# Optimization experiments

Measured on AMD Instinct MI355X. Metric: run time of the kernel, lower is better.

Reference implementation:

```python
import jax, jax.numpy as jnp
import numpy as np

D = 768
H = 12
DH = D // H


def setup_inputs() -> dict:
    key = jax.random.key(0)
    ks = jax.random.split(key, 7)
    B, S = 8, 1024
    sequences = jax.random.normal(ks[0], (B, S, D), dtype=jnp.float32)
    # per-head Linear params: weight [H, DH, DH] (torch Linear convention y = x W^T + b), bias [H, DH]
    scale = 1.0 / np.sqrt(DH)
    Wq = jax.random.uniform(ks[1], (H, DH, DH), jnp.float32, -scale, scale)
    Wk = jax.random.uniform(ks[2], (H, DH, DH), jnp.float32, -scale, scale)
    Wv = jax.random.uniform(ks[3], (H, DH, DH), jnp.float32, -scale, scale)
    bq = jax.random.uniform(ks[4], (H, DH), jnp.float32, -scale, scale)
    bk = jax.random.uniform(ks[5], (H, DH), jnp.float32, -scale, scale)
    bv = jax.random.uniform(ks[6], (H, DH), jnp.float32, -scale, scale)
    return {"sequences": sequences, "Wq": Wq, "Wk": Wk, "Wv": Wv,
            "bq": bq, "bk": bk, "bv": bv}


def reference(sequences, Wq, Wk, Wv, bq, bk, bv):
    B, S, _ = sequences.shape
    x = sequences.reshape(B, S, H, DH)  # head slices along feature dim
    # torch Linear: y = x @ W.T + b  ->  einsum over last dim of W
    Q = jnp.einsum('bshd,hed->bshe', x, Wq) + bq
    K = jnp.einsum('bshd,hed->bshe', x, Wk) + bk
    V = jnp.einsum('bshd,hed->bshe', x, Wv) + bv
    scores = jnp.einsum('bshe,bthe->bhst', Q, K) / np.sqrt(DH).astype(np.float32)
    attn = jax.nn.softmax(scores, axis=-1)  # [B,H,S,S]
    out = jnp.einsum('bhst,bthd->bshd', attn, V)
    return out.reshape(B, S, H * DH)
```

## Files before the change

### kernel.cpp

```cpp
#include <hip/hip_runtime.h>

#define NH 12
#define DHEAD 64
#define DMODEL 768
#define SEQ 1024
#define NBH 96

typedef _Float16 h8 __attribute__((ext_vector_type(8)));
typedef _Float16 h4 __attribute__((ext_vector_type(4)));
typedef __fp16   fp16x2 __attribute__((ext_vector_type(2)));
typedef float f32x4 __attribute__((ext_vector_type(4)));


__global__ __launch_bounds__(256) void proj_kernel(
    const float* __restrict__ x,
    const float* __restrict__ Wq, const float* __restrict__ Wk,
    const float* __restrict__ Wv,
    const float* __restrict__ bq, const float* __restrict__ bk,
    const float* __restrict__ bv,
    _Float16* __restrict__ Qf, _Float16* __restrict__ Kf,
    _Float16* __restrict__ Vf)
{
    __shared__ _Float16 xh[128][72];
    __shared__ _Float16 yh[128][72];

    const int h    = blockIdx.y;
    const int mtx  = blockIdx.z;
    const int tid  = threadIdx.x;
    const int row0 = blockIdx.x * 128;
    const int lane = tid & 63;
    const int w    = tid >> 6;
    const int g    = lane >> 4;
    const int r    = lane & 15;

    const int b    = row0 >> 10;
    const int bh   = b * NH + h;
    const int s16b = (row0 & 1023) >> 4;
    const int s32b = (row0 & 1023) >> 5;

#pragma unroll
    for (int p = 0; p < 8; ++p) {
        const int rr = p * 16 + (tid >> 4);
        const int c4 = (tid & 15) * 4;
        float4 v = *(const float4*)(x + (size_t)(row0 + rr) * DMODEL
                                      + h * DHEAD + c4);
        h4 o = { (_Float16)v.x, (_Float16)v.y, (_Float16)v.z, (_Float16)v.w };
        *(h4*)(&xh[rr][c4]) = o;
    }

    const float* W    = (mtx == 0 ? Wq : (mtx == 1 ? Wk : Wv)) + h * DHEAD * DHEAD;
    const float* bias = (mtx == 0 ? bq : (mtx == 1 ? bk : bv)) + h * DHEAD;
    const float  ws   = (mtx == 0) ? 0.125f * 1.44269504f : 1.0f;

    h8 bf[4][2];
    float bcol[4];
#pragma unroll
    for (int n = 0; n < 4; ++n) {
        const float* Wr = W + (n * 16 + r) * DHEAD;
#pragma unroll
        for (int hf = 0; hf < 2; ++hf) {
            const float* p = Wr + hf * 32 + g * 8;
            float4 w0 = *(const float4*)(p);
            float4 w1 = *(const float4*)(p + 4);
            h8 o = { (_Float16)(w0.x * ws), (_Float16)(w0.y * ws),
                     (_Float16)(w0.z * ws), (_Float16)(w0.w * ws),
                     (_Float16)(w1.x * ws), (_Float16)(w1.y * ws),
                     (_Float16)(w1.z * ws), (_Float16)(w1.w * ws) };
            bf[n][hf] = o;
        }
        bcol[n] = bias[n * 16 + r] * ws;
    }
    __syncthreads();

#pragma unroll
    for (int gg = 0; gg < 2; ++gg) {
        const int gi = w + gg * 4;
        const h8 af0 = *(const h8*)(&xh[gi * 16 + r][g * 8]);
        const h8 af1 = *(const h8*)(&xh[gi * 16 + r][32 + g * 8]);
#pragma unroll
        for (int n = 0; n < 4; ++n) {
            f32x4 d = { bcol[n], bcol[n], bcol[n], bcol[n] };
            d = __builtin_amdgcn_mfma_f32_16x16x32_f16(af0, bf[n][0], d, 0, 0, 0);
            d = __builtin_amdgcn_mfma_f32_16x16x32_f16(af1, bf[n][1], d, 0, 0, 0);
#pragma unroll
            for (int reg = 0; reg < 4; ++reg)
                yh[gi * 16 + g * 4 + reg][n * 16 + r] = (_Float16)d[reg];
        }
    }
    __syncthreads();

    if (mtx < 2) {
        const int s16l = tid >> 5;
        const int lx   = tid & 31;
        h8* dstb = (h8*)(mtx == 0 ? Qf : Kf)
                 + ((size_t)(bh * 64 + s16b + s16l)) * 128;
#pragma unroll
        for (int hf = 0; hf < 2; ++hf)
#pragma unroll
            for (int li = 0; li < 2; ++li) {
                const int ln  = lx + li * 32;
                const int gg2 = ln >> 4, rr2 = ln & 15;
                h8 v = *(const h8*)(&yh[s16l * 16 + rr2][hf * 32 + gg2 * 8]);
                dstb[hf * 64 + ln] = v;
            }
    } else {
        const int s32l = tid >> 6;
        const int t    = (tid >> 4) & 3;
        const int li   = tid & 15;
        h8 wv[4];
#pragma unroll
        for (int k = 0; k < 4; ++k) {
            const int ln  = li * 4 + k;
            const int gg2 = ln >> 4, rr2 = ln & 15;
#pragma unroll
            for (int j = 0; j < 4; ++j) {
                wv[k][j]     = yh[s32l * 32 +      gg2 * 4 + j][t * 16 + rr2];
                wv[k][j + 4] = yh[s32l * 32 + 16 + gg2 * 4 + j][t * 16 + rr2];
            }
        }
        h8* dst = (h8*)Vf
                + (((size_t)(bh * 32 + s32b + s32l)) * 4 + t) * 64 + li * 4;
#pragma unroll
        for (int k = 0; k < 4; ++k) dst[k] = wv[k];
    }
}

__global__ __launch_bounds__(256, 4) void attn_kernel(
    const _Float16* __restrict__ Qf, const _Float16* __restrict__ Kf,
    const _Float16* __restrict__ Vf, float* __restrict__ out)
{
    __shared__ _Float16 kbuf[4][2048];
    __shared__ _Float16 vbuf[4][2048];

    const int orig    = blockIdx.x;
    const int logical = (orig & 7) * 96 + (orig >> 3);
    const int bh      = logical >> 3;
    const int qblk    = logical & 7;
    const int tid  = threadIdx.x;
    const int lane = tid & 63;
    const int w    = tid >> 6;
    const int g    = lane >> 4;
    const int r    = lane & 15;

    const h8* Qb = (const h8*)Qf + (size_t)bh * 64 * 128;
    const h8* Kb = (const h8*)Kf + (size_t)bh * 64 * 128;
    const h8* Vb = (const h8*)Vf + (size_t)bh * 32 * 256;

    const int q16_0 = qblk * 8 + w * 2;

    h8 qf[2][2];
#pragma unroll
    for (int qg = 0; qg < 2; ++qg) {
        qf[qg][0] = Qb[(q16_0 + qg) * 128 + lane];
        qf[qg][1] = Qb[(q16_0 + qg) * 128 + 64 + lane];
    }
    asm volatile("s_waitcnt vmcnt(0)" ::: "memory");

    f32x4 ot[2][4] = {};
    float lsum[2] = {};

#define STAGE(c, buf)                                                         \
    {                                                                         \
        const h8* gk = Kb + (size_t)(c) * 256 + w * 64 + lane;                \
        const h8* gv = Vb + (size_t)(c) * 256 + w * 64 + lane;                \
        __builtin_amdgcn_global_load_lds(                                     \
            (const __attribute__((address_space(1))) void*)gk,                \
            (__attribute__((address_space(3))) void*)(&kbuf[buf][w * 512]),   \
            16, 0, 0);                                                        \
        __builtin_amdgcn_global_load_lds(                                     \
            (const __attribute__((address_space(1))) void*)gv,                \
            (__attribute__((address_space(3))) void*)(&vbuf[buf][w * 512]),   \
            16, 0, 0);                                                        \
    }

#define CHUNK(c, VM, DOSTAGE)                                                 \
    {                                                                         \
        if (DOSTAGE) STAGE((c) + 2, ((c) + 2) & 3)                            \
        asm volatile("s_waitcnt vmcnt(" #VM ")" ::: "memory");                \
        __builtin_amdgcn_s_barrier();                                         \
        const int cur = (c) & 3;                                              \
        __builtin_amdgcn_s_setprio(1);                                        \
        h8 kr0[2], kr1[2];                                                    \
        kr0[0] = *(const h8*)(&kbuf[cur][0 * 512 + lane * 8]);                \
        kr0[1] = *(const h8*)(&kbuf[cur][1 * 512 + lane * 8]);                \
        kr1[0] = *(const h8*)(&kbuf[cur][2 * 512 + lane * 8]);                \
        kr1[1] = *(const h8*)(&kbuf[cur][3 * 512 + lane * 8]);                \
        f32x4 s[2][2];                                                        \
        _Pragma("unroll")                                                     \
        for (int qg = 0; qg < 2; ++qg) {                                      \
            s[qg][0] = __builtin_amdgcn_mfma_f32_16x16x32_f16(                \
                kr0[0], qf[qg][0], (f32x4){0.f, 0.f, 0.f, 0.f}, 0, 0, 0);     \
            s[qg][0] = __builtin_amdgcn_mfma_f32_16x16x32_f16(                \
                kr0[1], qf[qg][1], s[qg][0], 0, 0, 0);                        \
            s[qg][1] = __builtin_amdgcn_mfma_f32_16x16x32_f16(                \
                kr1[0], qf[qg][0], (f32x4){0.f, 0.f, 0.f, 0.f}, 0, 0, 0);     \
            s[qg][1] = __builtin_amdgcn_mfma_f32_16x16x32_f16(                \
                kr1[1], qf[qg][1], s[qg][1], 0, 0, 0);                        \
        }                                                                     \
        h8 up[2];                                                             \
        _Pragma("unroll")                                                     \
        for (int qg = 0; qg < 2; ++qg) {                                      \
            float p0 = __builtin_amdgcn_exp2f(s[qg][0][0]);                   \
            float p1 = __builtin_amdgcn_exp2f(s[qg][0][1]);                   \
            float p2 = __builtin_amdgcn_exp2f(s[qg][0][2]);                   \
            float p3 = __builtin_amdgcn_exp2f(s[qg][0][3]);                   \
            float p4 = __builtin_amdgcn_exp2f(s[qg][1][0]);                   \
            float p5 = __builtin_amdgcn_exp2f(s[qg][1][1]);                   \
            float p6 = __builtin_amdgcn_exp2f(s[qg][1][2]);                   \
            float p7 = __builtin_amdgcn_exp2f(s[qg][1][3]);                   \
            lsum[qg] += ((p0 + p1) + (p2 + p3)) + ((p4 + p5) + (p6 + p7));    \
            union { fp16x2 v2[4]; h8 v8; } u;                                 \
            u.v2[0] = __builtin_amdgcn_cvt_pkrtz(p0, p1);                     \
            u.v2[1] = __builtin_amdgcn_cvt_pkrtz(p2, p3);                     \
            u.v2[2] = __builtin_amdgcn_cvt_pkrtz(p4, p5);                     \
            u.v2[3] = __builtin_amdgcn_cvt_pkrtz(p6, p7);                     \
            up[qg] = u.v8;                                                    \
        }                                                                     \
        _Pragma("unroll")                                                     \
        for (int t = 0; t < 4; ++t) {                                         \
            h8 vr = *(const h8*)(&vbuf[cur][t * 512 + lane * 8]);             \
            ot[0][t] = __builtin_amdgcn_mfma_f32_16x16x32_f16(                \
                vr, up[0], ot[0][t], 0, 0, 0);                                \
            ot[1][t] = __builtin_amdgcn_mfma_f32_16x16x32_f16(                \
                vr, up[1], ot[1][t], 0, 0, 0);                                \
        }                                                                     \
        __builtin_amdgcn_s_setprio(0);                                        \
    }

    STAGE(0, 0)
    STAGE(1, 1)

    CHUNK(0, 4, 1)  CHUNK(1, 4, 1)  CHUNK(2, 4, 1)  CHUNK(3, 4, 1)
    CHUNK(4, 4, 1)  CHUNK(5, 4, 1)  CHUNK(6, 4, 1)  CHUNK(7, 4, 1)
    CHUNK(8, 4, 1)  CHUNK(9, 4, 1)  CHUNK(10, 4, 1) CHUNK(11, 4, 1)
    CHUNK(12, 4, 1) CHUNK(13, 4, 1) CHUNK(14, 4, 1) CHUNK(15, 4, 1)
    CHUNK(16, 4, 1) CHUNK(17, 4, 1) CHUNK(18, 4, 1) CHUNK(19, 4, 1)
    CHUNK(20, 4, 1) CHUNK(21, 4, 1) CHUNK(22, 4, 1) CHUNK(23, 4, 1)
    CHUNK(24, 4, 1) CHUNK(25, 4, 1) CHUNK(26, 4, 1) CHUNK(27, 4, 1)
    CHUNK(28, 4, 1) CHUNK(29, 4, 1) CHUNK(30, 2, 0) CHUNK(31, 0, 0)
#undef CHUNK
#undef STAGE

    const int b = bh / NH, h = bh % NH;
#pragma unroll
    for (int qg = 0; qg < 2; ++qg) {
        float l = lsum[qg];
        l += __shfl_xor(l, 16);
        l += __shfl_xor(l, 32);
        const float inv = 1.0f / l;
        float* op = out + ((size_t)b * SEQ + (q16_0 + qg) * 16 + r) * DMODEL
                  + h * DHEAD + g * 4;
#pragma unroll
        for (int t = 0; t < 4; ++t) {
            float4 res = { ot[qg][t][0] * inv, ot[qg][t][1] * inv,
                           ot[qg][t][2] * inv, ot[qg][t][3] * inv };
            *(float4*)(op + t * 16) = res;
        }
    }
}

extern "C" void kernel_launch(void* const* d_in, const int* in_sizes, int n_in,
                              void* d_out, int out_size, void* d_ws, size_t ws_size,
                              hipStream_t stream)
{
    const float* x  = (const float*)d_in[0];
    const float* Wq = (const float*)d_in[1];
    const float* Wk = (const float*)d_in[2];
    const float* Wv = (const float*)d_in[3];
    const float* bq = (const float*)d_in[4];
    const float* bk = (const float*)d_in[5];
    const float* bv = (const float*)d_in[6];
    float* out = (float*)d_out;

    const size_t frag_elems = (size_t)NBH * 64 * 2 * 64 * 8;
    _Float16* Qf = (_Float16*)d_ws;
    _Float16* Kf = Qf + frag_elems;
    _Float16* Vf = Kf + frag_elems;

    proj_kernel<<<dim3(64, 12, 3), 256, 0, stream>>>(x, Wq, Wk, Wv, bq, bk, bv,
                                                     Qf, Kf, Vf);
    attn_kernel<<<768, 256, 0, stream>>>(Qf, Kf, Vf, out);
}
```

Baseline: 65.19 us.

## Split attention key range across two wave groups per block with LDS reduction

Doubles the attention block to 512 threads, where each pair of waves splits the key sequence in half (split-K style) and each half processes 16 chunks instead of 32. Partial outputs and row sums from the second half are combined through shared memory before normalisation and store. The LDS pipeline changes from a 4-buffer to a 3-buffer ring per half, and staging now happens after the barrier. This shortens each wave's serial dependency chain and raises the number of resident waves, at the cost of an extra reduction pass and more LDS per block.

Result: slower. 90.27 us (+38.5%).

```diff
diff --git a/kernel.cpp b/kernel.cpp
--- a/kernel.cpp
+++ b/kernel.cpp
@@ -125,12 +125,12 @@
     }
 }
 
-__global__ __launch_bounds__(256, 4) void attn_kernel(
+__global__ __launch_bounds__(512, 6) void attn_kernel(
     const _Float16* __restrict__ Qf, const _Float16* __restrict__ Kf,
     const _Float16* __restrict__ Vf, float* __restrict__ out)
 {
-    __shared__ _Float16 kbuf[4][2048];
-    __shared__ _Float16 vbuf[4][2048];
+    __shared__ __align__(16) char smem[49152];
+    __shared__ float lred[4][2][16];
 
     const int orig    = blockIdx.x;
     const int logical = (orig & 7) * 96 + (orig >> 3);
@@ -139,14 +139,16 @@
     const int tid  = threadIdx.x;
     const int lane = tid & 63;
     const int w    = tid >> 6;
+    const int qh   = w >> 1;
+    const int kq   = w & 1;
     const int g    = lane >> 4;
     const int r    = lane & 15;
 
     const h8* Qb = (const h8*)Qf + (size_t)bh * 64 * 128;
-    const h8* Kb = (const h8*)Kf + (size_t)bh * 64 * 128;
-    const h8* Vb = (const h8*)Vf + (size_t)bh * 32 * 256;
-
-    const int q16_0 = qblk * 8 + w * 2;
+    const h8* Ks = (const h8*)Kf + (size_t)bh * 64 * 128 + (size_t)kq * 4096;
+    const h8* Vs = (const h8*)Vf + (size_t)bh * 32 * 256 + (size_t)kq * 4096;
+
+    const int q16_0 = qblk * 8 + qh * 2;
 
     h8 qf[2][2];
 #pragma unroll
@@ -159,32 +161,35 @@
     f32x4 ot[2][4] = {};
     float lsum[2] = {};
 
-#define STAGE(c, buf)                                                         \
+#define SBASE(bfi) (smem + kq * 24576 + (bfi) * 8192)
+
+#define STAGE(c, bfi)                                                         \
     {                                                                         \
-        const h8* gk = Kb + (size_t)(c) * 256 + w * 64 + lane;                \
-        const h8* gv = Vb + (size_t)(c) * 256 + w * 64 + lane;                \
+        const h8* gk = Ks + (size_t)(c) * 256 + qh * 64 + lane;               \
+        const h8* gv = Vs + (size_t)(c) * 256 + qh * 64 + lane;               \
         __builtin_amdgcn_global_load_lds(                                     \
             (const __attribute__((address_space(1))) void*)gk,                \
-            (__attribute__((address_space(3))) void*)(&kbuf[buf][w * 512]),   \
+            (__attribute__((address_space(3))) void*)(SBASE(bfi) + qh * 1024),\
             16, 0, 0);                                                        \
         __builtin_amdgcn_global_load_lds(                                     \
             (const __attribute__((address_space(1))) void*)gv,                \
-            (__attribute__((address_space(3))) void*)(&vbuf[buf][w * 512]),   \
+            (__attribute__((address_space(3))) void*)(SBASE(bfi) + 4096       \
+                                                      + qh * 1024),           \
             16, 0, 0);                                                        \
     }
 
 #define CHUNK(c, VM, DOSTAGE)                                                 \
     {                                                                         \
-        if (DOSTAGE) STAGE((c) + 2, ((c) + 2) & 3)                            \
         asm volatile("s_waitcnt vmcnt(" #VM ")" ::: "memory");                \
         __builtin_amdgcn_s_barrier();                                         \
-        const int cur = (c) & 3;                                              \
+        if (DOSTAGE) STAGE((c) + 2, ((c) + 2) % 3)                            \
+        const _Float16* cb = (const _Float16*)SBASE((c) % 3);                 \
         __builtin_amdgcn_s_setprio(1);                                        \
         h8 kr0[2], kr1[2];                                                    \
-        kr0[0] = *(const h8*)(&kbuf[cur][0 * 512 + lane * 8]);                \
-        kr0[1] = *(const h8*)(&kbuf[cur][1 * 512 + lane * 8]);                \
-        kr1[0] = *(const h8*)(&kbuf[cur][2 * 512 + lane * 8]);                \
-        kr1[1] = *(const h8*)(&kbuf[cur][3 * 512 + lane * 8]);                \
+        kr0[0] = *(const h8*)(cb + lane * 8);                                 \
+        kr0[1] = *(const h8*)(cb + 512 + lane * 8);                           \
+        kr1[0] = *(const h8*)(cb + 1024 + lane * 8);                          \
+        kr1[1] = *(const h8*)(cb + 1536 + lane * 8);                          \
         f32x4 s[2][2];                                                        \
         _Pragma("unroll")                                                     \
         for (int qg = 0; qg < 2; ++qg) {                                      \
@@ -218,7 +223,7 @@
         }                                                                     \
         _Pragma("unroll")                                                     \
         for (int t = 0; t < 4; ++t) {                                         \
-            h8 vr = *(const h8*)(&vbuf[cur][t * 512 + lane * 8]);             \
+            h8 vr = *(const h8*)(cb + 2048 + t * 512 + lane * 8);             \
             ot[0][t] = __builtin_amdgcn_mfma_f32_16x16x32_f16(                \
                 vr, up[0], ot[0][t], 0, 0, 0);                                \
             ot[1][t] = __builtin_amdgcn_mfma_f32_16x16x32_f16(                \
@@ -230,31 +235,46 @@
     STAGE(0, 0)
     STAGE(1, 1)
 
-    CHUNK(0, 4, 1)  CHUNK(1, 4, 1)  CHUNK(2, 4, 1)  CHUNK(3, 4, 1)
-    CHUNK(4, 4, 1)  CHUNK(5, 4, 1)  CHUNK(6, 4, 1)  CHUNK(7, 4, 1)
-    CHUNK(8, 4, 1)  CHUNK(9, 4, 1)  CHUNK(10, 4, 1) CHUNK(11, 4, 1)
-    CHUNK(12, 4, 1) CHUNK(13, 4, 1) CHUNK(14, 4, 1) CHUNK(15, 4, 1)
-    CHUNK(16, 4, 1) CHUNK(17, 4, 1) CHUNK(18, 4, 1) CHUNK(19, 4, 1)
-    CHUNK(20, 4, 1) CHUNK(21, 4, 1) CHUNK(22, 4, 1) CHUNK(23, 4, 1)
-    CHUNK(24, 4, 1) CHUNK(25, 4, 1) CHUNK(26, 4, 1) CHUNK(27, 4, 1)
-    CHUNK(28, 4, 1) CHUNK(29, 4, 1) CHUNK(30, 2, 0) CHUNK(31, 0, 0)
+    CHUNK(0, 2, 1)  CHUNK(1, 2, 1)  CHUNK(2, 2, 1)  CHUNK(3, 2, 1)
+    CHUNK(4, 2, 1)  CHUNK(5, 2, 1)  CHUNK(6, 2, 1)  CHUNK(7, 2, 1)
+    CHUNK(8, 2, 1)  CHUNK(9, 2, 1)  CHUNK(10, 2, 1) CHUNK(11, 2, 1)
+    CHUNK(12, 2, 1) CHUNK(13, 2, 1) CHUNK(14, 2, 0) CHUNK(15, 0, 0)
 #undef CHUNK
 #undef STAGE
-
-    const int b = bh / NH, h = bh % NH;
+#undef SBASE
+
 #pragma unroll
     for (int qg = 0; qg < 2; ++qg) {
-        float l = lsum[qg];
-        l += __shfl_xor(l, 16);
-        l += __shfl_xor(l, 32);
-        const float inv = 1.0f / l;
-        float* op = out + ((size_t)b * SEQ + (q16_0 + qg) * 16 + r) * DMODEL
-                  + h * DHEAD + g * 4;
-#pragma unroll
-        for (int t = 0; t < 4; ++t) {
-            float4 res = { ot[qg][t][0] * inv, ot[qg][t][1] * inv,
-                           ot[qg][t][2] * inv, ot[qg][t][3] * inv };
-            *(float4*)(op + t * 16) = res;
+        lsum[qg] += __shfl_xor(lsum[qg], 16);
+        lsum[qg] += __shfl_xor(lsum[qg], 32);
+    }
+
+    f32x4* osum = (f32x4*)smem;
+    __syncthreads();
+    if (kq == 1) {
+#pragma unroll
+        for (int qg = 0; qg < 2; ++qg) {
+#pragma unroll
+            for (int t = 0; t < 4; ++t)
+                osum[((qh * 2 + qg) * 4 + t) * 64 + lane] = ot[qg][t];
+            if (g == 0) lred[qh][qg][r] = lsum[qg];
+        }
+    }
+    __syncthreads();
+    if (kq == 0) {
+        const int b = bh / NH, h = bh % NH;
+#pragma unroll
+        for (int qg = 0; qg < 2; ++qg) {
+            const float tot = lsum[qg] + lred[qh][qg][r];
+            const float inv = 1.0f / tot;
+            float* op = out + ((size_t)b * SEQ + (q16_0 + qg) * 16 + r) * DMODEL
+                      + h * DHEAD + g * 4;
+#pragma unroll
+            for (int t = 0; t < 4; ++t) {
+                f32x4 o = ot[qg][t] + osum[((qh * 2 + qg) * 4 + t) * 64 + lane];
+                float4 res = { o[0] * inv, o[1] * inv, o[2] * inv, o[3] * inv };
+                *(float4*)(op + t * 16) = res;
+            }
         }
     }
 }
@@ -279,5 +299,5 @@
 
     proj_kernel<<<dim3(64, 12, 3), 256, 0, stream>>>(x, Wq, Wk, Wv, bq, bk, bv,
                                                      Qf, Kf, Vf);
-    attn_kernel<<<768, 256, 0, stream>>>(Qf, Kf, Vf, out);
+    attn_kernel<<<768, 512, 0, stream>>>(Qf, Kf, Vf, out);
 }
```
